# Optimization experiments

Hardware: AMD Instinct MI355X
Metric: run time of the kernel (lower is better)

Reference implementation:

```python
import jax, jax.numpy as jnp
import numpy as np

N_NODES = 50000


def gcn_conv(x, src, dst, W, b, n_nodes):
    """PyG GCNConv: add self-loops, sym-normalize, aggregate, linear.
    x' = D^{-1/2} (A + I) D^{-1/2} X W + b
    """
    loop = jnp.arange(n_nodes, dtype=src.dtype)
    s = jnp.concatenate([src, loop])  # [E + N]
    d = jnp.concatenate([dst, loop])
    h = x @ W  # [N, out]
    deg = jax.ops.segment_sum(jnp.ones_like(d, dtype=h.dtype), d, num_segments=n_nodes)
    dinv = jnp.where(deg > 0, jax.lax.rsqrt(deg), 0.0)
    norm = dinv[s] * dinv[d]  # [E + N]
    msg = h[s] * norm[:, None]  # gather + scale (edge-level, memory bound)
    out = jax.ops.segment_sum(msg, d, num_segments=n_nodes)
    return out + b


def setup_inputs() -> dict:
    key = jax.random.key(0)
    k1, k2, k3, k4 = jax.random.split(key, 4)
    n, e, d_in, d_hid, d_out = N_NODES, 800000, 128, 128, 64
    x = jax.random.normal(k1, (n, d_in), dtype=jnp.float32)
    edge_index = jax.random.randint(k2, (2, e), 0, n, dtype=jnp.int64)
    W1 = jax.random.normal(k3, (d_in, d_hid), dtype=jnp.float32) * (1.0 / np.sqrt(d_in))
    b1 = jnp.zeros((d_hid,), dtype=jnp.float32)
    W2 = jax.random.normal(k4, (d_hid, d_out), dtype=jnp.float32) * (1.0 / np.sqrt(d_hid))
    b2 = jnp.zeros((d_out,), dtype=jnp.float32)
    return {"x": x, "edge_index": edge_index, "W1": W1, "b1": b1, "W2": W2, "b2": b2}


def reference(x, edge_index, W1, b1, W2, b2):
    src, dst = edge_index[0], edge_index[1]
    h = gcn_conv(x, src, dst, W1, b1, N_NODES)
    h = jax.nn.relu(h)
    h = gcn_conv(h, src, dst, W2, b2, N_NODES)
    # edge-wise gather + dot product -> per-edge logits [E]
    logits = jnp.sum(h[src] * h[dst], axis=-1)
    return logits
```

## Files before the change

kernel.cpp:

```cpp
#include <hip/hip_runtime.h>
#include <hip/hip_bf16.h>


using ushort_t = unsigned short;

__global__ void cnt_rank_k(const int* __restrict__ dst, int* __restrict__ cnt,
                           int* __restrict__ rank, int E) {
    int t = blockIdx.x * blockDim.x + threadIdx.x;
    int e = t * 4;
    if (e + 4 <= E) {
        int4 d4 = *reinterpret_cast<const int4*>(dst + e);
        int4 r4;
        r4.x = atomicAdd(&cnt[d4.x], 1);
        r4.y = atomicAdd(&cnt[d4.y], 1);
        r4.z = atomicAdd(&cnt[d4.z], 1);
        r4.w = atomicAdd(&cnt[d4.w], 1);
        *reinterpret_cast<int4*>(rank + e) = r4;
    } else {
        for (int i = e; i < E; i++) rank[i] = atomicAdd(&cnt[dst[i]], 1);
    }
}

__global__ void scan1_k(const int* __restrict__ cnt, int* __restrict__ incl,
                        int* __restrict__ bsum, int N) {
    __shared__ int sh[256];
    int i = blockIdx.x * 256 + threadIdx.x;
    int v = (i < N) ? cnt[i] : 0;
    sh[threadIdx.x] = v;
    __syncthreads();
#pragma unroll
    for (int off = 1; off < 256; off <<= 1) {
        int t = (threadIdx.x >= off) ? sh[threadIdx.x - off] : 0;
        __syncthreads();
        sh[threadIdx.x] += t;
        __syncthreads();
    }
    if (i < N) incl[i] = sh[threadIdx.x];
    if (threadIdx.x == 255) bsum[blockIdx.x] = sh[255];
}

__global__ __launch_bounds__(256) void scan23_k(const int* __restrict__ cnt,
                                                const int* __restrict__ incl,
                                                const int* __restrict__ bsum,
                                                int* __restrict__ rowptr,
                                                float* __restrict__ dinv,
                                                int N, int E, int NB) {
    __shared__ int sh[256];
    __shared__ int blockOff;
    int v = (threadIdx.x < NB) ? bsum[threadIdx.x] : 0;
    sh[threadIdx.x] = v;
    __syncthreads();
#pragma unroll
    for (int off = 1; off < 256; off <<= 1) {
        int t = (threadIdx.x >= off) ? sh[threadIdx.x - off] : 0;
        __syncthreads();
        sh[threadIdx.x] += t;
        __syncthreads();
    }
    if (threadIdx.x == blockIdx.x) blockOff = sh[threadIdx.x] - v;
    __syncthreads();
    int i = blockIdx.x * 256 + threadIdx.x;
    if (i < N) {
        int c = cnt[i];
        rowptr[i] = incl[i] - c + blockOff;
        dinv[i] = rsqrtf(1.0f + (float)c);
    }
    if (i == 0) rowptr[N] = E;
}

template <int BN, bool RELU>
__device__ __forceinline__ void gemm_body32(const float* __restrict__ A,
                                            const float* __restrict__ W,
                                            const float* __restrict__ dscale,
                                            float4* __restrict__ OutT,
                                            int M, int Nn, int row0,
                                            float (*As)[36], float (*Bs)[BN]) {
    constexpr int K = 128, BK = 16;
    constexpr int TN = BN / 16;
    const int tid = threadIdx.x;
    const int tx = tid & 15, ty = tid >> 4;

    float acc[2][TN];
#pragma unroll
    for (int m = 0; m < 2; m++)
#pragma unroll
        for (int n = 0; n < TN; n++) acc[m][n] = 0.0f;

    for (int kt = 0; kt < K; kt += BK) {
        if (tid < 128) {
            int r = tid >> 2;
            int kq = (tid & 3) * 4;
            float4 av = make_float4(0.f, 0.f, 0.f, 0.f);
            int gr = row0 + r;
            if (gr < M)
                av = *reinterpret_cast<const float4*>(A + (size_t)gr * K + kt + kq);
            if (RELU) {
                av.x = fmaxf(av.x, 0.f); av.y = fmaxf(av.y, 0.f);
                av.z = fmaxf(av.z, 0.f); av.w = fmaxf(av.w, 0.f);
            }
            As[kq + 0][r] = av.x; As[kq + 1][r] = av.y;
            As[kq + 2][r] = av.z; As[kq + 3][r] = av.w;
        }
#pragma unroll
        for (int s = 0; s < (BK * BN) / (256 * 4); s++) {
            int f = s * 256 + tid;
            int brow = f / (BN / 4);
            int bcol = (f % (BN / 4)) * 4;
            float4 bv = *reinterpret_cast<const float4*>(W + (size_t)(kt + brow) * BN + bcol);
            *reinterpret_cast<float4*>(&Bs[brow][bcol]) = bv;
        }
        __syncthreads();

#pragma unroll
        for (int k = 0; k < BK; k++) {
            float2 a2 = *reinterpret_cast<const float2*>(&As[k][ty * 2]);
            float a[2] = {a2.x, a2.y};
            float b[TN];
            float4 b0 = *reinterpret_cast<const float4*>(&Bs[k][tx * 4]);
            b[0] = b0.x; b[1] = b0.y; b[2] = b0.z; b[3] = b0.w;
            if (TN == 8) {
                float4 b1 = *reinterpret_cast<const float4*>(&Bs[k][64 + tx * 4]);
                b[4] = b1.x; b[5] = b1.y; b[6] = b1.z; b[7] = b1.w;
            }
#pragma unroll
            for (int m = 0; m < 2; m++)
#pragma unroll
                for (int n = 0; n < TN; n++) acc[m][n] = fmaf(a[m], b[n], acc[m][n]);
        }
        __syncthreads();
    }

    const int chunk0 = tx >> 2;
    const int off = tx & 3;
#pragma unroll
    for (int m = 0; m < 2; m++) {
        int gr = row0 + ty * 2 + m;
        if (gr < M) {
            float dv = dscale[gr];
            float4 o0 = make_float4(acc[m][0] * dv, acc[m][1] * dv,
                                    acc[m][2] * dv, acc[m][3] * dv);
            OutT[((size_t)chunk0 * Nn + gr) * 4 + off] = o0;
            if (TN == 8) {
                float4 o1 = make_float4(acc[m][4] * dv, acc[m][5] * dv,
                                        acc[m][6] * dv, acc[m][7] * dv);
                OutT[((size_t)(4 + chunk0) * Nn + gr) * 4 + off] = o1;
            }
        }
    }
}

__global__ __launch_bounds__(256) void gemm1_fill_k(const float* __restrict__ A,
                                                    const float* __restrict__ W,
                                                    const float* __restrict__ dscale,
                                                    float4* __restrict__ OutT,
                                                    int M, int Nn,
                                                    const int* __restrict__ src,
                                                    const int* __restrict__ dst,
                                                    const int* __restrict__ rowptr,
                                                    const int* __restrict__ rank,
                                                    ushort_t* __restrict__ colu, int E,
                                                    int gemmBlocks) {
    __shared__ float As[16][36];
    __shared__ float Bs[16][128];
    int g = (int)blockIdx.x;
    if (g >= gemmBlocks) {
        int t = (g - gemmBlocks) * 256 + threadIdx.x;
        int e = t * 4;
        if (e + 4 <= E) {
            int4 s4 = *reinterpret_cast<const int4*>(src + e);
            int4 d4 = *reinterpret_cast<const int4*>(dst + e);
            int4 r4 = *reinterpret_cast<const int4*>(rank + e);
            colu[rowptr[d4.x] + r4.x] = (ushort_t)s4.x;
            colu[rowptr[d4.y] + r4.y] = (ushort_t)s4.y;
            colu[rowptr[d4.z] + r4.z] = (ushort_t)s4.z;
            colu[rowptr[d4.w] + r4.w] = (ushort_t)s4.w;
        } else {
            for (int i = e; i < E; i++)
                colu[rowptr[dst[i]] + rank[i]] = (ushort_t)src[i];
        }
        return;
    }
    gemm_body32<128, false>(A, W, dscale, OutT, M, Nn, g * 32, As, Bs);
}

__global__ __launch_bounds__(256) void gemm2_k(const float* __restrict__ A,
                                               const float* __restrict__ W,
                                               const float* __restrict__ dscale,
                                               float4* __restrict__ OutT,
                                               int M, int Nn) {
    __shared__ float As[16][36];
    __shared__ float Bs[16][64];
    gemm_body32<64, true>(A, W, dscale, OutT, M, Nn, (int)blockIdx.x * 32, As, Bs);
}

__device__ __forceinline__ float4 pull_body(const int* __restrict__ rowptr,
                                            const ushort_t* __restrict__ colu,
                                            const float4* __restrict__ T,
                                            size_t cb, int v, int j) {
    int p0 = rowptr[v], p1 = rowptr[v + 1];
    float4 acc = T[(cb + v) * 4 + j];
    int p = p0;

    if (p + 8 <= p1) {
        int n0 = colu[p + 0], n1 = colu[p + 1], n2 = colu[p + 2], n3 = colu[p + 3];
        int n4 = colu[p + 4], n5 = colu[p + 5], n6 = colu[p + 6], n7 = colu[p + 7];
        for (;;) {
            bool nxt = (p + 16 <= p1);
            int m0, m1, m2, m3, m4, m5, m6, m7;
            if (nxt) {
                m0 = colu[p + 8];  m1 = colu[p + 9];  m2 = colu[p + 10]; m3 = colu[p + 11];
                m4 = colu[p + 12]; m5 = colu[p + 13]; m6 = colu[p + 14]; m7 = colu[p + 15];
            }
            float4 g0 = T[(cb + n0) * 4 + j];
            float4 g1 = T[(cb + n1) * 4 + j];
            float4 g2 = T[(cb + n2) * 4 + j];
            float4 g3 = T[(cb + n3) * 4 + j];
            float4 g4 = T[(cb + n4) * 4 + j];
            float4 g5 = T[(cb + n5) * 4 + j];
            float4 g6 = T[(cb + n6) * 4 + j];
            float4 g7 = T[(cb + n7) * 4 + j];
            acc.x += ((g0.x + g1.x) + (g2.x + g3.x)) + ((g4.x + g5.x) + (g6.x + g7.x));
            acc.y += ((g0.y + g1.y) + (g2.y + g3.y)) + ((g4.y + g5.y) + (g6.y + g7.y));
            acc.z += ((g0.z + g1.z) + (g2.z + g3.z)) + ((g4.z + g5.z) + (g6.z + g7.z));
            acc.w += ((g0.w + g1.w) + (g2.w + g3.w)) + ((g4.w + g5.w) + (g6.w + g7.w));
            p += 8;
            if (!nxt) break;
            n0 = m0; n1 = m1; n2 = m2; n3 = m3;
            n4 = m4; n5 = m5; n6 = m6; n7 = m7;
        }
    }
    for (; p + 4 <= p1; p += 4) {
        int u0 = colu[p], u1 = colu[p + 1], u2 = colu[p + 2], u3 = colu[p + 3];
        float4 a = T[(cb + u0) * 4 + j];
        float4 b = T[(cb + u1) * 4 + j];
        float4 c = T[(cb + u2) * 4 + j];
        float4 d = T[(cb + u3) * 4 + j];
        acc.x += (a.x + b.x) + (c.x + d.x);
        acc.y += (a.y + b.y) + (c.y + d.y);
        acc.z += (a.z + b.z) + (c.z + d.z);
        acc.w += (a.w + b.w) + (c.w + d.w);
    }
    for (; p < p1; p++) {
        float4 a = T[(cb + colu[p]) * 4 + j];
        acc.x += a.x; acc.y += a.y; acc.z += a.z; acc.w += a.w;
    }
    return acc;
}

__global__ __launch_bounds__(256) void pull128c_k(const int* __restrict__ rowptr,
                                                  const ushort_t* __restrict__ colu,
                                                  const float4* __restrict__ hsT,
                                                  const float* __restrict__ dinv,
                                                  const float4* __restrict__ bias4,
                                                  float4* __restrict__ out4, int N) {
    int c = (int)(blockIdx.x & 7);
    int g = (int)(blockIdx.x >> 3);
    int v = g * 64 + (int)(threadIdx.x >> 2);
    if (v >= N) return;
    int j = threadIdx.x & 3;
    float4 acc = pull_body(rowptr, colu, hsT, (size_t)c * N, v, j);
    float dv = dinv[v];
    float4 bv = bias4[c * 4 + j];
    out4[(size_t)v * 32 + c * 4 + j] =
        make_float4(fmaf(acc.x, dv, bv.x), fmaf(acc.y, dv, bv.y),
                    fmaf(acc.z, dv, bv.z), fmaf(acc.w, dv, bv.w));
}

__global__ __launch_bounds__(256) void pull64c_k(const int* __restrict__ rowptr,
                                                 const ushort_t* __restrict__ colu,
                                                 const float4* __restrict__ g2T,
                                                 const float* __restrict__ dinv,
                                                 const float4* __restrict__ bias4,
                                                 float4* __restrict__ outT, int N) {
    int c = (int)(blockIdx.x & 3);
    int g = (int)(blockIdx.x >> 2);
    int v = g * 64 + (int)(threadIdx.x >> 2);
    if (v >= N) return;
    int j = threadIdx.x & 3;
    size_t cb = (size_t)c * N;
    float4 acc = pull_body(rowptr, colu, g2T, cb, v, j);
    float dv = dinv[v];
    float4 bv = bias4[c * 4 + j];
    outT[(cb + v) * 4 + j] =
        make_float4(fmaf(acc.x, dv, bv.x), fmaf(acc.y, dv, bv.y),
                    fmaf(acc.z, dv, bv.z), fmaf(acc.w, dv, bv.w));
}

__global__ __launch_bounds__(256) void logits_part_k(const int* __restrict__ src,
                                                     const int* __restrict__ dst,
                                                     const float4* __restrict__ aggT,
                                                     float* __restrict__ part,
                                                     int N, int E) {
    int c = (int)(blockIdx.x & 3);
    int blk = (int)(blockIdx.x >> 2);
    int g = (int)(threadIdx.x >> 2);
    int j = threadIdx.x & 3;
    size_t cb = (size_t)c * N;
    int ebase = blk * 256;

#pragma unroll
    for (int i = 0; i < 4; i++) {
        int e = ebase + i * 64 + g;
        if (e < E) {
            int s = src[e], d = dst[e];
            float4 a = aggT[(cb + s) * 4 + j];
            float4 b = aggT[(cb + d) * 4 + j];
            float t = a.x * b.x + a.y * b.y + a.z * b.z + a.w * b.w;
            t += __shfl_xor(t, 1);
            t += __shfl_xor(t, 2);
            if (j == 0) part[(size_t)c * E + e] = t;
        }
    }
}

__global__ __launch_bounds__(256) void logits_reduce_k(const float* __restrict__ part,
                                                       float* __restrict__ out, int E) {
    int i = blockIdx.x * blockDim.x + threadIdx.x;
    int e4 = E >> 2;
    if (i < e4) {
        const float4* p0 = reinterpret_cast<const float4*>(part);
        const float4* p1 = reinterpret_cast<const float4*>(part + (size_t)E);
        const float4* p2 = reinterpret_cast<const float4*>(part + (size_t)E * 2);
        const float4* p3 = reinterpret_cast<const float4*>(part + (size_t)E * 3);
        float4 a = p0[i], b = p1[i], c = p2[i], d = p3[i];
        float4 o = make_float4((a.x + b.x) + (c.x + d.x), (a.y + b.y) + (c.y + d.y),
                               (a.z + b.z) + (c.z + d.z), (a.w + b.w) + (c.w + d.w));
        reinterpret_cast<float4*>(out)[i] = o;
    }
    if (blockIdx.x == 0 && threadIdx.x < (E & 3)) {
        int e = e4 * 4 + threadIdx.x;
        out[e] = part[e] + part[(size_t)E + e] + part[(size_t)E * 2 + e] +
                 part[(size_t)E * 3 + e];
    }
}

extern "C" void kernel_launch(void* const* d_in, const int* in_sizes, int n_in,
                              void* d_out, int out_size, void* d_ws, size_t ws_size,
                              hipStream_t stream) {
    const float* x  = (const float*)d_in[0];
    const int* ei   = (const int*)d_in[1];
    const float* W1 = (const float*)d_in[2];
    const float* b1 = (const float*)d_in[3];
    const float* W2 = (const float*)d_in[4];
    const float* b2 = (const float*)d_in[5];
    float* out = (float*)d_out;

    const int N = in_sizes[0] / 128;
    const int E = in_sizes[1] / 2;
    const int* src = ei;
    const int* dst = ei + E;

    float* ws    = (float*)d_ws;
    float* dinv  = ws;
    float* bufA  = ws + 50176;
    float* bufB  = bufA + (size_t)N * 128;
    float* hsT   = bufA;
    float* agg1  = bufB;
    float* g2T   = bufA;
    float* agg2T = bufA + (size_t)N * 64;
    float* part  = bufB;

    int* ibase  = (int*)(bufB + (size_t)N * 128);
    int* cnt    = ibase;
    int* incl   = cnt + N;
    int* rowptr = incl + N;
    int* bsum   = rowptr + (N + 1);
    int* rank   = bsum + 256;
    ushort_t* colu = (ushort_t*)(rank + E);

    const int B = 256;
    const int NB = (N + 255) / 256;
    const unsigned ng64 = (unsigned)((N + 63) / 64);

    hipMemsetAsync(cnt, 0, (size_t)N * sizeof(int), stream);
    cnt_rank_k<<<(E / 4 + B - 1) / B, B, 0, stream>>>(dst, cnt, rank, E);
    scan1_k<<<NB, 256, 0, stream>>>(cnt, incl, bsum, N);
    scan23_k<<<NB, 256, 0, stream>>>(cnt, incl, bsum, rowptr, dinv, N, E, NB);

    {
        int gemmBlocks = (N + 31) / 32;
        int fillBlocks = (E / 4 + B - 1) / B;
        gemm1_fill_k<<<gemmBlocks + fillBlocks, 256, 0, stream>>>(
            x, W1, dinv, (float4*)hsT, N, N, src, dst, rowptr, rank, colu, E,
            gemmBlocks);
    }

    pull128c_k<<<ng64 * 8, 256, 0, stream>>>(rowptr, colu, (const float4*)hsT, dinv,
                                             (const float4*)b1, (float4*)agg1, N);

    gemm2_k<<<(N + 31) / 32, 256, 0, stream>>>(agg1, W2, dinv, (float4*)g2T, N, N);

    pull64c_k<<<ng64 * 4, 256, 0, stream>>>(rowptr, colu, (const float4*)g2T, dinv,
                                            (const float4*)b2, (float4*)agg2T, N);

    {
        unsigned blk = (unsigned)((E + 255) / 256);
        logits_part_k<<<blk * 4, 256, 0, stream>>>(src, dst, (const float4*)agg2T,
                                                   part, N, E);
        unsigned rblk = (unsigned)((E / 4 + 255) / 256);
        logits_reduce_k<<<rblk, 256, 0, stream>>>(part, out, E);
    }
}
```

Measured before the change: 215.7 us.

## Sort nodes by in-degree to balance work in pull aggregation kernels

Builds a degree histogram during the scan, prefix-sums it in a new single-block kernel, and scatters node ids into a degree-sorted permutation. Both pull aggregation kernels then process nodes in this order, so that nodes with similar degree share a wavefront and the loop divergence between lanes drops. In exchange it adds one extra launch plus histogram atomics, and output writes and rowptr reads become scattered and less coalesced.

```diff
diff --git a/kernel.cpp b/kernel.cpp
--- a/kernel.cpp
+++ b/kernel.cpp
@@ -22,7 +22,7 @@
 }
 
 __global__ void scan1_k(const int* __restrict__ cnt, int* __restrict__ incl,
-                        int* __restrict__ bsum, int N) {
+                        int* __restrict__ bsum, int* __restrict__ hist, int N) {
     __shared__ int sh[256];
     int i = blockIdx.x * 256 + threadIdx.x;
     int v = (i < N) ? cnt[i] : 0;
@@ -35,8 +35,27 @@
         sh[threadIdx.x] += t;
         __syncthreads();
     }
-    if (i < N) incl[i] = sh[threadIdx.x];
+    if (i < N) {
+        incl[i] = sh[threadIdx.x];
+        atomicAdd(&hist[min(v, 1023)], 1);
+    }
     if (threadIdx.x == 255) bsum[blockIdx.x] = sh[255];
+}
+
+__global__ __launch_bounds__(1024) void hscan_k(const int* __restrict__ hist,
+                                                int* __restrict__ hcur) {
+    __shared__ int sh[1024];
+    int v = hist[threadIdx.x];
+    sh[threadIdx.x] = v;
+    __syncthreads();
+#pragma unroll
+    for (int off = 1; off < 1024; off <<= 1) {
+        int t = (threadIdx.x >= off) ? sh[threadIdx.x - off] : 0;
+        __syncthreads();
+        sh[threadIdx.x] += t;
+        __syncthreads();
+    }
+    hcur[threadIdx.x] = sh[threadIdx.x] - v;
 }
 
 __global__ __launch_bounds__(256) void scan23_k(const int* __restrict__ cnt,
@@ -44,6 +63,8 @@
                                                 const int* __restrict__ bsum,
                                                 int* __restrict__ rowptr,
                                                 float* __restrict__ dinv,
+                                                int* __restrict__ hcur,
+                                                int* __restrict__ perm,
                                                 int N, int E, int NB) {
     __shared__ int sh[256];
     __shared__ int blockOff;
@@ -64,6 +85,8 @@
         int c = cnt[i];
         rowptr[i] = incl[i] - c + blockOff;
         dinv[i] = rsqrtf(1.0f + (float)c);
+        int pos = atomicAdd(&hcur[min(c, 1023)], 1);
+        perm[pos] = i;
     }
     if (i == 0) rowptr[N] = E;
 }
@@ -249,14 +272,16 @@
 
 __global__ __launch_bounds__(256) void pull128c_k(const int* __restrict__ rowptr,
                                                   const ushort_t* __restrict__ colu,
+                                                  const int* __restrict__ perm,
                                                   const float4* __restrict__ hsT,
                                                   const float* __restrict__ dinv,
                                                   const float4* __restrict__ bias4,
                                                   float4* __restrict__ out4, int N) {
     int c = (int)(blockIdx.x & 7);
     int g = (int)(blockIdx.x >> 3);
-    int v = g * 64 + (int)(threadIdx.x >> 2);
-    if (v >= N) return;
+    int idx = g * 64 + (int)(threadIdx.x >> 2);
+    if (idx >= N) return;
+    int v = perm[idx];
     int j = threadIdx.x & 3;
     float4 acc = pull_body(rowptr, colu, hsT, (size_t)c * N, v, j);
     float dv = dinv[v];
@@ -268,14 +293,16 @@
 
 __global__ __launch_bounds__(256) void pull64c_k(const int* __restrict__ rowptr,
                                                  const ushort_t* __restrict__ colu,
+                                                 const int* __restrict__ perm,
                                                  const float4* __restrict__ g2T,
                                                  const float* __restrict__ dinv,
                                                  const float4* __restrict__ bias4,
                                                  float4* __restrict__ outT, int N) {
     int c = (int)(blockIdx.x & 3);
     int g = (int)(blockIdx.x >> 2);
-    int v = g * 64 + (int)(threadIdx.x >> 2);
-    if (v >= N) return;
+    int idx = g * 64 + (int)(threadIdx.x >> 2);
+    if (idx >= N) return;
+    int v = perm[idx];
     int j = threadIdx.x & 3;
     size_t cb = (size_t)c * N;
     float4 acc = pull_body(rowptr, colu, g2T, cb, v, j);
@@ -362,20 +389,24 @@
 
     int* ibase  = (int*)(bufB + (size_t)N * 128);
     int* cnt    = ibase;
-    int* incl   = cnt + N;
+    int* hist   = cnt + N;
+    int* hcur   = hist + 1024;
+    int* incl   = hcur + 1024;
     int* rowptr = incl + N;
     int* bsum   = rowptr + (N + 1);
-    int* rank   = bsum + 256;
+    int* perm   = bsum + 256;
+    int* rank   = perm + N;
     ushort_t* colu = (ushort_t*)(rank + E);
 
     const int B = 256;
     const int NB = (N + 255) / 256;
     const unsigned ng64 = (unsigned)((N + 63) / 64);
 
-    hipMemsetAsync(cnt, 0, (size_t)N * sizeof(int), stream);
+    hipMemsetAsync(cnt, 0, ((size_t)N + 1024) * sizeof(int), stream);
     cnt_rank_k<<<(E / 4 + B - 1) / B, B, 0, stream>>>(dst, cnt, rank, E);
-    scan1_k<<<NB, 256, 0, stream>>>(cnt, incl, bsum, N);
-    scan23_k<<<NB, 256, 0, stream>>>(cnt, incl, bsum, rowptr, dinv, N, E, NB);
+    scan1_k<<<NB, 256, 0, stream>>>(cnt, incl, bsum, hist, N);
+    hscan_k<<<1, 1024, 0, stream>>>(hist, hcur);
+    scan23_k<<<NB, 256, 0, stream>>>(cnt, incl, bsum, rowptr, dinv, hcur, perm, N, E, NB);
 
     {
         int gemmBlocks = (N + 31) / 32;
@@ -385,13 +416,13 @@
             gemmBlocks);
     }
 
-    pull128c_k<<<ng64 * 8, 256, 0, stream>>>(rowptr, colu, (const float4*)hsT, dinv,
-                                             (const float4*)b1, (float4*)agg1, N);
+    pull128c_k<<<ng64 * 8, 256, 0, stream>>>(rowptr, colu, perm, (const float4*)hsT,
+                                             dinv, (const float4*)b1, (float4*)agg1, N);
 
     gemm2_k<<<(N + 31) / 32, 256, 0, stream>>>(agg1, W2, dinv, (float4*)g2T, N, N);
 
-    pull64c_k<<<ng64 * 4, 256, 0, stream>>>(rowptr, colu, (const float4*)g2T, dinv,
-                                            (const float4*)b2, (float4*)agg2T, N);
+    pull64c_k<<<ng64 * 4, 256, 0, stream>>>(rowptr, colu, perm, (const float4*)g2T,
+                                            dinv, (const float4*)b2, (float4*)agg2T, N);
 
     {
         unsigned blk = (unsigned)((E + 255) / 256);
```

Measured after the change: 446.9 us. 107% more time.

## Pad CSR rows to multiples of eight with a zero dummy node

Applied to the files above, without the earlier changes.

Each CSR row is padded to a multiple of eight entries, and the padding slots point at an extra all-zero row appended to the transformed feature buffers. The pull loop can then fetch neighbour indices as aligned 16-byte vectors and handle eight neighbours per iteration with no remainder loops. This removes tail handling and scalar index loads from the gather. In exchange it adds padded gathers, which are extra wasted memory traffic for rows of average degree about 17, plus a small cost to write the padding and zero the dummy rows.

```diff
diff --git a/kernel.cpp b/kernel.cpp
--- a/kernel.cpp
+++ b/kernel.cpp
@@ -25,7 +25,7 @@
                         int* __restrict__ bsum, int N) {
     __shared__ int sh[256];
     int i = blockIdx.x * 256 + threadIdx.x;
-    int v = (i < N) ? cnt[i] : 0;
+    int v = (i < N) ? ((cnt[i] + 7) & ~7) : 0;
     sh[threadIdx.x] = v;
     __syncthreads();
 #pragma unroll
@@ -44,9 +44,10 @@
                                                 const int* __restrict__ bsum,
                                                 int* __restrict__ rowptr,
                                                 float* __restrict__ dinv,
-                                                int N, int E, int NB) {
+                                                ushort_t* __restrict__ colu,
+                                                int N, int NB) {
     __shared__ int sh[256];
-    __shared__ int blockOff;
+    __shared__ int blockOff, totalPad;
     int v = (threadIdx.x < NB) ? bsum[threadIdx.x] : 0;
     sh[threadIdx.x] = v;
     __syncthreads();
@@ -58,14 +59,18 @@
         __syncthreads();
     }
     if (threadIdx.x == blockIdx.x) blockOff = sh[threadIdx.x] - v;
+    if (threadIdx.x == NB - 1) totalPad = sh[threadIdx.x];
     __syncthreads();
     int i = blockIdx.x * 256 + threadIdx.x;
     if (i < N) {
         int c = cnt[i];
-        rowptr[i] = incl[i] - c + blockOff;
+        int cp = (c + 7) & ~7;
+        int excl = incl[i] - cp + blockOff;
+        rowptr[i] = excl;
         dinv[i] = rsqrtf(1.0f + (float)c);
-    }
-    if (i == 0) rowptr[N] = E;
+        for (int k = c; k < cp; k++) colu[excl + k] = (ushort_t)N;
+    }
+    if (i == 0) rowptr[N] = totalPad;
 }
 
 template <int BN, bool RELU>
@@ -73,7 +78,7 @@
                                             const float* __restrict__ W,
                                             const float* __restrict__ dscale,
                                             float4* __restrict__ OutT,
-                                            int M, int Nn, int row0,
+                                            int M, int Np, int row0,
                                             float (*As)[36], float (*Bs)[BN]) {
     constexpr int K = 128, BK = 16;
     constexpr int TN = BN / 16;
@@ -139,11 +144,11 @@
             float dv = dscale[gr];
             float4 o0 = make_float4(acc[m][0] * dv, acc[m][1] * dv,
                                     acc[m][2] * dv, acc[m][3] * dv);
-            OutT[((size_t)chunk0 * Nn + gr) * 4 + off] = o0;
+            OutT[((size_t)chunk0 * Np + gr) * 4 + off] = o0;
             if (TN == 8) {
                 float4 o1 = make_float4(acc[m][4] * dv, acc[m][5] * dv,
                                         acc[m][6] * dv, acc[m][7] * dv);
-                OutT[((size_t)(4 + chunk0) * Nn + gr) * 4 + off] = o1;
+                OutT[((size_t)(4 + chunk0) * Np + gr) * 4 + off] = o1;
             }
         }
     }
@@ -153,7 +158,7 @@
                                                     const float* __restrict__ W,
                                                     const float* __restrict__ dscale,
                                                     float4* __restrict__ OutT,
-                                                    int M, int Nn,
+                                                    int M, int Np,
                                                     const int* __restrict__ src,
                                                     const int* __restrict__ dst,
                                                     const int* __restrict__ rowptr,
@@ -180,17 +185,25 @@
         }
         return;
     }
-    gemm_body32<128, false>(A, W, dscale, OutT, M, Nn, g * 32, As, Bs);
+    if (g == 0 && threadIdx.x < 32) {
+        int c = threadIdx.x >> 2, q4 = threadIdx.x & 3;
+        OutT[((size_t)c * Np + (Np - 1)) * 4 + q4] = make_float4(0.f, 0.f, 0.f, 0.f);
+    }
+    gemm_body32<128, false>(A, W, dscale, OutT, M, Np, g * 32, As, Bs);
 }
 
 __global__ __launch_bounds__(256) void gemm2_k(const float* __restrict__ A,
                                                const float* __restrict__ W,
                                                const float* __restrict__ dscale,
                                                float4* __restrict__ OutT,
-                                               int M, int Nn) {
+                                               int M, int Np) {
     __shared__ float As[16][36];
     __shared__ float Bs[16][64];
-    gemm_body32<64, true>(A, W, dscale, OutT, M, Nn, (int)blockIdx.x * 32, As, Bs);
+    if (blockIdx.x == 0 && threadIdx.x < 16) {
+        int c = threadIdx.x >> 2, q4 = threadIdx.x & 3;
+        OutT[((size_t)c * Np + (Np - 1)) * 4 + q4] = make_float4(0.f, 0.f, 0.f, 0.f);
+    }
+    gemm_body32<64, true>(A, W, dscale, OutT, M, Np, (int)blockIdx.x * 32, As, Bs);
 }
 
 __device__ __forceinline__ float4 pull_body(const int* __restrict__ rowptr,
@@ -199,50 +212,32 @@
                                             size_t cb, int v, int j) {
     int p0 = rowptr[v], p1 = rowptr[v + 1];
     float4 acc = T[(cb + v) * 4 + j];
-    int p = p0;
-
-    if (p + 8 <= p1) {
-        int n0 = colu[p + 0], n1 = colu[p + 1], n2 = colu[p + 2], n3 = colu[p + 3];
-        int n4 = colu[p + 4], n5 = colu[p + 5], n6 = colu[p + 6], n7 = colu[p + 7];
-        for (;;) {
-            bool nxt = (p + 16 <= p1);
-            int m0, m1, m2, m3, m4, m5, m6, m7;
-            if (nxt) {
-                m0 = colu[p + 8];  m1 = colu[p + 9];  m2 = colu[p + 10]; m3 = colu[p + 11];
-                m4 = colu[p + 12]; m5 = colu[p + 13]; m6 = colu[p + 14]; m7 = colu[p + 15];
-            }
-            float4 g0 = T[(cb + n0) * 4 + j];
-            float4 g1 = T[(cb + n1) * 4 + j];
-            float4 g2 = T[(cb + n2) * 4 + j];
-            float4 g3 = T[(cb + n3) * 4 + j];
-            float4 g4 = T[(cb + n4) * 4 + j];
-            float4 g5 = T[(cb + n5) * 4 + j];
-            float4 g6 = T[(cb + n6) * 4 + j];
-            float4 g7 = T[(cb + n7) * 4 + j];
-            acc.x += ((g0.x + g1.x) + (g2.x + g3.x)) + ((g4.x + g5.x) + (g6.x + g7.x));
-            acc.y += ((g0.y + g1.y) + (g2.y + g3.y)) + ((g4.y + g5.y) + (g6.y + g7.y));
-            acc.z += ((g0.z + g1.z) + (g2.z + g3.z)) + ((g4.z + g5.z) + (g6.z + g7.z));
-            acc.w += ((g0.w + g1.w) + (g2.w + g3.w)) + ((g4.w + g5.w) + (g6.w + g7.w));
-            p += 8;
-            if (!nxt) break;
-            n0 = m0; n1 = m1; n2 = m2; n3 = m3;
-            n4 = m4; n5 = m5; n6 = m6; n7 = m7;
-        }
-    }
-    for (; p + 4 <= p1; p += 4) {
-        int u0 = colu[p], u1 = colu[p + 1], u2 = colu[p + 2], u3 = colu[p + 3];
-        float4 a = T[(cb + u0) * 4 + j];
-        float4 b = T[(cb + u1) * 4 + j];
-        float4 c = T[(cb + u2) * 4 + j];
-        float4 d = T[(cb + u3) * 4 + j];
-        acc.x += (a.x + b.x) + (c.x + d.x);
-        acc.y += (a.y + b.y) + (c.y + d.y);
-        acc.z += (a.z + b.z) + (c.z + d.z);
-        acc.w += (a.w + b.w) + (c.w + d.w);
-    }
-    for (; p < p1; p++) {
-        float4 a = T[(cb + colu[p]) * 4 + j];
-        acc.x += a.x; acc.y += a.y; acc.z += a.z; acc.w += a.w;
+    int nb = (p1 - p0) >> 3;
+    if (nb == 0) return acc;
+
+    const uint4* cp = reinterpret_cast<const uint4*>(colu + p0);
+    uint4 ci = cp[0];
+    for (int ib = 0; ib < nb; ib++) {
+        bool more = (ib + 1 < nb);
+        uint4 cn;
+        if (more) cn = cp[ib + 1];
+        int n0 = ci.x & 0xFFFF, n1 = ci.x >> 16;
+        int n2 = ci.y & 0xFFFF, n3 = ci.y >> 16;
+        int n4 = ci.z & 0xFFFF, n5 = ci.z >> 16;
+        int n6 = ci.w & 0xFFFF, n7 = ci.w >> 16;
+        float4 g0 = T[(cb + n0) * 4 + j];
+        float4 g1 = T[(cb + n1) * 4 + j];
+        float4 g2 = T[(cb + n2) * 4 + j];
+        float4 g3 = T[(cb + n3) * 4 + j];
+        float4 g4 = T[(cb + n4) * 4 + j];
+        float4 g5 = T[(cb + n5) * 4 + j];
+        float4 g6 = T[(cb + n6) * 4 + j];
+        float4 g7 = T[(cb + n7) * 4 + j];
+        acc.x += ((g0.x + g1.x) + (g2.x + g3.x)) + ((g4.x + g5.x) + (g6.x + g7.x));
+        acc.y += ((g0.y + g1.y) + (g2.y + g3.y)) + ((g4.y + g5.y) + (g6.y + g7.y));
+        acc.z += ((g0.z + g1.z) + (g2.z + g3.z)) + ((g4.z + g5.z) + (g6.z + g7.z));
+        acc.w += ((g0.w + g1.w) + (g2.w + g3.w)) + ((g4.w + g5.w) + (g6.w + g7.w));
+        ci = cn;
     }
     return acc;
 }
@@ -252,13 +247,14 @@
                                                   const float4* __restrict__ hsT,
                                                   const float* __restrict__ dinv,
                                                   const float4* __restrict__ bias4,
-                                                  float4* __restrict__ out4, int N) {
+                                                  float4* __restrict__ out4,
+                                                  int N, int Np) {
     int c = (int)(blockIdx.x & 7);
     int g = (int)(blockIdx.x >> 3);
     int v = g * 64 + (int)(threadIdx.x >> 2);
     if (v >= N) return;
     int j = threadIdx.x & 3;
-    float4 acc = pull_body(rowptr, colu, hsT, (size_t)c * N, v, j);
+    float4 acc = pull_body(rowptr, colu, hsT, (size_t)c * Np, v, j);
     float dv = dinv[v];
     float4 bv = bias4[c * 4 + j];
     out4[(size_t)v * 32 + c * 4 + j] =
@@ -271,17 +267,17 @@
                                                  const float4* __restrict__ g2T,
                                                  const float* __restrict__ dinv,
                                                  const float4* __restrict__ bias4,
-                                                 float4* __restrict__ outT, int N) {
+                                                 float4* __restrict__ outT,
+                                                 int N, int Np) {
     int c = (int)(blockIdx.x & 3);
     int g = (int)(blockIdx.x >> 2);
     int v = g * 64 + (int)(threadIdx.x >> 2);
     if (v >= N) return;
     int j = threadIdx.x & 3;
-    size_t cb = (size_t)c * N;
-    float4 acc = pull_body(rowptr, colu, g2T, cb, v, j);
+    float4 acc = pull_body(rowptr, colu, g2T, (size_t)c * Np, v, j);
     float dv = dinv[v];
     float4 bv = bias4[c * 4 + j];
-    outT[(cb + v) * 4 + j] =
+    outT[((size_t)c * N + v) * 4 + j] =
         make_float4(fmaf(acc.x, dv, bv.x), fmaf(acc.y, dv, bv.y),
                     fmaf(acc.z, dv, bv.z), fmaf(acc.w, dv, bv.w));
 }
@@ -347,26 +343,27 @@
 
     const int N = in_sizes[0] / 128;
     const int E = in_sizes[1] / 2;
+    const int Np = N + 1;
     const int* src = ei;
     const int* dst = ei + E;
 
-    float* ws    = (float*)d_ws;
-    float* dinv  = ws;
-    float* bufA  = ws + 50176;
-    float* bufB  = bufA + (size_t)N * 128;
-    float* hsT   = bufA;
-    float* agg1  = bufB;
-    float* g2T   = bufA;
-    float* agg2T = bufA + (size_t)N * 64;
-    float* part  = bufB;
-
-    int* ibase  = (int*)(bufB + (size_t)N * 128);
+    float* ws      = (float*)d_ws;
+    float* dinv    = ws;
+    float* regionA = ws + 50176;
+    float* regionB = regionA + (size_t)Np * 128;
+    float* hsT     = regionA;
+    float* g2T     = regionA;
+    float* agg2T   = regionA + (size_t)4 * Np * 16;
+    float* agg1    = regionB;
+    float* part    = regionB;
+
+    int* ibase  = (int*)(regionB + (size_t)N * 128);
     int* cnt    = ibase;
     int* incl   = cnt + N;
     int* rowptr = incl + N;
     int* bsum   = rowptr + (N + 1);
     int* rank   = bsum + 256;
-    ushort_t* colu = (ushort_t*)(rank + E);
+    ushort_t* colu = (ushort_t*)(((uintptr_t)(rank + E) + 15) & ~(uintptr_t)15);
 
     const int B = 256;
     const int NB = (N + 255) / 256;
@@ -375,23 +372,25 @@
     hipMemsetAsync(cnt, 0, (size_t)N * sizeof(int), stream);
     cnt_rank_k<<<(E / 4 + B - 1) / B, B, 0, stream>>>(dst, cnt, rank, E);
     scan1_k<<<NB, 256, 0, stream>>>(cnt, incl, bsum, N);
-    scan23_k<<<NB, 256, 0, stream>>>(cnt, incl, bsum, rowptr, dinv, N, E, NB);
+    scan23_k<<<NB, 256, 0, stream>>>(cnt, incl, bsum, rowptr, dinv, colu, N, NB);
 
     {
         int gemmBlocks = (N + 31) / 32;
         int fillBlocks = (E / 4 + B - 1) / B;
         gemm1_fill_k<<<gemmBlocks + fillBlocks, 256, 0, stream>>>(
-            x, W1, dinv, (float4*)hsT, N, N, src, dst, rowptr, rank, colu, E,
+            x, W1, dinv, (float4*)hsT, N, Np, src, dst, rowptr, rank, colu, E,
             gemmBlocks);
     }
 
-    pull128c_k<<<ng64 * 8, 256, 0, stream>>>(rowptr, colu, (const float4*)hsT, dinv,
-                                             (const float4*)b1, (float4*)agg1, N);
-
-    gemm2_k<<<(N + 31) / 32, 256, 0, stream>>>(agg1, W2, dinv, (float4*)g2T, N, N);
-
-    pull64c_k<<<ng64 * 4, 256, 0, stream>>>(rowptr, colu, (const float4*)g2T, dinv,
-                                            (const float4*)b2, (float4*)agg2T, N);
+    pull128c_k<<<ng64 * 8, 256, 0, stream>>>(rowptr, colu, (const float4*)hsT,
+                                             dinv, (const float4*)b1,
+                                             (float4*)agg1, N, Np);
+
+    gemm2_k<<<(N + 31) / 32, 256, 0, stream>>>(agg1, W2, dinv, (float4*)g2T, N, Np);
+
+    pull64c_k<<<ng64 * 4, 256, 0, stream>>>(rowptr, colu, (const float4*)g2T,
+                                            dinv, (const float4*)b2,
+                                            (float4*)agg2T, N, Np);
 
     {
         unsigned blk = (unsigned)((E + 255) / 256);
```

After: 212.9 us. About the same (-1.3%).
